# Kernel tuning notes

Hardware: AMD Instinct MI355X
Metric: run time of the kernel (lower is better)

## Reference

```python
import jax, jax.numpy as jnp
import numpy as np

# dims
B, N, T, D = 32, 207, 12, 128
H, HD, L, FF = 8, 16, 4, 512
PL, OD, IN = 12, 1, 1
SCALE = 1.0 / float(np.sqrt(HD))
NEG = -1e9


def ln(x, g, b, eps=1e-5):
    m = jnp.mean(x, -1, keepdims=True)
    v = jnp.mean((x - m) ** 2, -1, keepdims=True)
    return (x - m) * jax.lax.rsqrt(v + eps) * g + b


def setup_inputs() -> dict:
    key = jax.random.key(0)
    keys = iter(jax.random.split(key, 48))
    def rn(shape, s=0.02):
        return jax.random.normal(next(keys), shape, jnp.float32) * s
    z = lambda *s: jnp.zeros(s, jnp.float32)
    o = lambda *s: jnp.ones(s, jnp.float32)
    inp = {
        "x": jax.random.normal(next(keys), (B, N, T, IN), jnp.float32),
        "adj": jax.random.randint(next(keys), (N, N), 0, 2, jnp.int32),
        "Wi": rn((IN, D)), "bi": z(D),
        # spatial blocks (stacked over L layers)
        "Wq": rn((L, D, D)), "Wk": rn((L, D, D)), "Wv": rn((L, D, D)),
        "Wo": rn((L, D, D)), "bo": z(L, D),
        "sW1": rn((L, D, FF)), "sB1": z(L, FF), "sW2": rn((L, FF, D)), "sB2": z(L, D),
        "sg1": o(L, D), "sh1": z(L, D), "sg2": o(L, D), "sh2": z(L, D),
        # temporal blocks
        "Win": rn((L, D, 3 * D)), "Bin": z(L, 3 * D), "Wout": rn((L, D, D)), "Bout": z(L, D),
        "tW1": rn((L, D, FF)), "tB1": z(L, FF), "tW2": rn((L, FF, D)), "tB2": z(L, D),
        "tg1": o(L, D), "th1": z(L, D), "tg2": o(L, D), "th2": z(L, D),
        # prediction head
        "P1": rn((D, 2 * D)), "Pb1": z(2 * D), "P2": rn((2 * D, D)), "Pb2": z(D),
        "P3": rn((D, PL * OD)), "Pb3": z(PL * OD),
    }
    return inp


def reference(x, adj, Wi, bi, Wq, Wk, Wv, Wo, bo, sW1, sB1, sW2, sB2,
              sg1, sh1, sg2, sh2, Win, Bin, Wout, Bout, tW1, tB1, tW2, tB2,
              tg1, th1, tg2, th2, P1, Pb1, P2, Pb2, P3, Pb3):
    mask = (adj == 0)  # [N,N] True = masked (no edge)
    cmask = jnp.triu(jnp.ones((T, T), bool), 1)  # causal mask over time
    h = x @ Wi + bi  # [B,N,T,D]
    for l in range(L):
        # --- spatial adjacency-masked attention (vectorized over t) ---
        xn = ln(h, sg1[l], sh1[l])
        q = (xn @ Wq[l]).reshape(B, N, T, H, HD)
        k = (xn @ Wk[l]).reshape(B, N, T, H, HD)
        v = (xn @ Wv[l]).reshape(B, N, T, H, HD)
        sc = jnp.einsum('bnthd,bmthd->bthnm', q, k) * SCALE  # [B,T,H,N,N]
        sc = jnp.where(mask[None, None, None], NEG, sc)
        a = jax.nn.softmax(sc, -1)
        o = jnp.einsum('bthnm,bmthd->bnthd', a, v).reshape(B, N, T, D)
        h = h + o @ Wo[l] + bo[l]
        xn = ln(h, sg2[l], sh2[l])
        h = h + jax.nn.relu(xn @ sW1[l] + sB1[l]) @ sW2[l] + sB2[l]
        # --- temporal causal attention (per node) ---
        xn = ln(h, tg1[l], th1[l])
        qkv = xn @ Win[l] + Bin[l]
        q, k, v = jnp.split(qkv, 3, -1)
        q = q.reshape(B, N, T, H, HD)
        k = k.reshape(B, N, T, H, HD)
        v = v.reshape(B, N, T, H, HD)
        sc = jnp.einsum('bnthd,bnshd->bnhts', q, k) * SCALE  # [B,N,H,T,T]
        sc = jnp.where(cmask[None, None, None], NEG, sc)
        a = jax.nn.softmax(sc, -1)
        o = jnp.einsum('bnhts,bnshd->bnthd', a, v).reshape(B, N, T, D)
        h = h + o @ Wout[l] + Bout[l]
        xn = ln(h, tg2[l], th2[l])
        h = h + jax.nn.relu(xn @ tW1[l] + tB1[l]) @ tW2[l] + tB2[l]
    # prediction head on last time step
    hl = h[:, :, -1, :]  # [B,N,D]
    zz = jax.nn.relu(hl @ P1 + Pb1)
    zz = jax.nn.relu(zz @ P2 + Pb2)
    return (zz @ P3 + Pb3).reshape(B, N, PL, OD)
```

## Files before the change

kernel.cpp:

```cpp
#include <hip/hip_runtime.h>
#include <hip/hip_bf16.h>

#define B_   32
#define N_   207
#define T_   12
#define D_   128
#define H_   8
#define HD_  16
#define L_   4
#define FF_  512
#define PL_  12
#define TOK  (B_*N_*T_)
#define ROWS2 (B_*N_)
#define SCALE_ 0.25f
#define NEG_  -1e9f
#define NPAD 208
#define KQ2  24
#define KVH  232
#define SLAB 3312
#define MSK_N (13*13*256)

typedef __hip_bfloat16 bf16;
typedef unsigned int u32;
typedef __attribute__((ext_vector_type(8))) short bf16x8;
typedef __attribute__((ext_vector_type(8))) _Float16 f16x8;
typedef __attribute__((ext_vector_type(4))) float f32x4;

__device__ __forceinline__ float b2f(bf16 x){ return __bfloat162float(x); }
__device__ __forceinline__ bf16  f2b(float x){ return __float2bfloat16(x); }

__device__ __forceinline__ void gll16(const bf16* g, bf16* l){
  __builtin_amdgcn_global_load_lds((const __attribute__((address_space(1))) void*)g,
                                   (__attribute__((address_space(3))) void*)l, 16, 0, 0);
}

__global__ void detect_k(const void* x, int* flag){
  __shared__ int cnt[256];
  const unsigned short* u = (const unsigned short*)x;
  int ok = 0;
  for (int i = threadIdx.x; i < 4096; i += 256){
    unsigned int bits = ((unsigned int)u[i]) << 16;
    float f = __uint_as_float(bits);
    float a = fabsf(f);
    if (f == 0.0f || (a > 1e-4f && a < 64.0f)) ok++;
  }
  cnt[threadIdx.x] = ok;
  __syncthreads();
  for (int s = 128; s > 0; s >>= 1){
    if (threadIdx.x < s) cnt[threadIdx.x] += cnt[threadIdx.x + s];
    __syncthreads();
  }
  if (threadIdx.x == 0) *flag = (cnt[0] > 3686) ? 1 : 0;
}

struct FlatArgs {
  const void* src[24];
  long long dst[24];
  int cum[25];
};
__global__ void cvt_flat_k(FlatArgs a, bf16* base, const int* flag, int total){
  int i = blockIdx.x*256 + threadIdx.x;
  if (i >= total) return;
  int j = 0;
  while (i >= a.cum[j+1]) j++;
  int loc = i - a.cum[j];
  float v = (*flag) ? b2f(((const bf16*)a.src[j])[loc]) : ((const float*)a.src[j])[loc];
  base[a.dst[j] + loc] = f2b(v);
}

struct TArgs {
  const void* src[10];
  long long dst[10];
  int K[10], Nc[10], Lstr[10], ro[10];
  float scale[10];
  int cum[11];
};
__global__ void cvt_t_k(TArgs a, bf16* base, const int* flag, int total){
  int i = blockIdx.x*256 + threadIdx.x;
  if (i >= total) return;
  int j = 0;
  while (i >= a.cum[j+1]) j++;
  int loc = i - a.cum[j];
  int KN = a.K[j]*a.Nc[j];
  int l = loc / KN; int rm = loc - l*KN; int k = rm / a.Nc[j]; int n = rm - k*a.Nc[j];
  float v = (*flag) ? b2f(((const bf16*)a.src[j])[loc]) : ((const float*)a.src[j])[loc];
  base[a.dst[j] + (long long)l*a.Lstr[j] + (long long)(a.ro[j]+n)*a.K[j] + k] = f2b(v*a.scale[j]);
}

__global__ void maskc_k(const int* adj, float* maskg){
  int i = blockIdx.x*256 + threadIdx.x;
  if (i >= MSK_N) return;
  int cell = i >> 8;
  int mi = cell / 13, nj = cell - mi*13;
  int rem = i & 255;
  int lane = rem >> 2, r = rem & 3;
  int quad = lane >> 4, cl = lane & 15;
  int row = mi*16 + quad*4 + r; if (row > 206) row = 206;
  int col = nj*16 + cl;
  float v;
  if (col > 206) v = -1e30f;
  else v = adj[row*N_ + col] ? 0.0f : NEG_;
  maskg[i] = v;
}

__global__ void embed_ln_k(const bf16* x, const bf16* Wi, const bf16* bi,
                           const bf16* g, const bf16* bta, float* h, bf16* xnb){
  int wave = threadIdx.x >> 6, lane = threadIdx.x & 63;
  int tok = blockIdx.x*4 + wave;
  if (tok >= TOK) return;
  float xv = b2f(x[tok]);
  float v0 = xv*b2f(Wi[lane])    + b2f(bi[lane]);
  float v1 = xv*b2f(Wi[lane+64]) + b2f(bi[lane+64]);
  float* hp = h + (size_t)tok*D_;
  hp[lane] = v0; hp[lane+64] = v1;
  float s = v0 + v1;
  for (int off = 32; off >= 1; off >>= 1) s += __shfl_xor(s, off, 64);
  float m = s * (1.0f/128.0f);
  float d0 = v0 - m, d1 = v1 - m;
  float vv = d0*d0 + d1*d1;
  for (int off = 32; off >= 1; off >>= 1) vv += __shfl_xor(vv, off, 64);
  float r = rsqrtf(vv*(1.0f/128.0f) + 1e-5f);
  bf16* op = xnb + (size_t)tok*D_;
  op[lane]    = f2b(d0*r*b2f(g[lane])    + b2f(bta[lane]));
  op[lane+64] = f2b(d1*r*b2f(g[lane+64]) + b2f(bta[lane+64]));
}

__global__ __launch_bounds__(256) void mgemm_k(const bf16* __restrict__ A,
    const bf16* __restrict__ Wt, const bf16* __restrict__ bias,
    bf16* __restrict__ outp, int ldo, int Ktot, int relu){
  __shared__ __align__(16) bf16 As[128*32];
  __shared__ __align__(16) bf16 Bs[128*32];
  int tid = threadIdx.x;
  int rowBase = blockIdx.y * 128, colBase = blockIdx.x * 128;
  int w = tid >> 6, lane = tid & 63, quad = lane >> 4, cl = lane & 15;
  int waveM = w >> 1, waveN = w & 1;
  f32x4 accr[4][4];
  #pragma unroll
  for (int i = 0; i < 4; i++)
    #pragma unroll
    for (int j = 0; j < 4; j++) accr[i][j] = (f32x4){0.f,0.f,0.f,0.f};
  int lr = tid >> 2, kc = tid & 3;
  const bf16* Ap = A  + (size_t)(rowBase + lr)*Ktot + kc*8;
  const bf16* Bp = Wt + (size_t)(colBase + lr)*Ktot + kc*8;
  bf16* AsW = As + tid*8;
  bf16* BsW = Bs + tid*8;
  for (int kk = 0; kk < Ktot; kk += 32){
    __syncthreads();
    gll16(Ap + kk, AsW);
    gll16(Ap + (size_t)64*Ktot + kk, AsW + 64*32);
    gll16(Bp + kk, BsW);
    gll16(Bp + (size_t)64*Ktot + kk, BsW + 64*32);
    __syncthreads();
    bf16x8 af[4], bfr[4];
    #pragma unroll
    for (int mi = 0; mi < 4; mi++)
      af[mi] = *(const bf16x8*)(As + (waveM*64 + mi*16 + cl)*32 + quad*8);
    #pragma unroll
    for (int nj = 0; nj < 4; nj++)
      bfr[nj] = *(const bf16x8*)(Bs + (waveN*64 + nj*16 + cl)*32 + quad*8);
    #pragma unroll
    for (int mi = 0; mi < 4; mi++)
      #pragma unroll
      for (int nj = 0; nj < 4; nj++)
        accr[mi][nj] = __builtin_amdgcn_mfma_f32_16x16x32_bf16(af[mi], bfr[nj], accr[mi][nj], 0,0,0);
  }
  float bv[4];
  #pragma unroll
  for (int nj = 0; nj < 4; nj++)
    bv[nj] = bias ? b2f(bias[colBase + waveN*64 + nj*16 + cl]) : 0.0f;
  #pragma unroll
  for (int mi = 0; mi < 4; mi++){
    int row0 = rowBase + waveM*64 + mi*16 + quad*4;
    #pragma unroll
    for (int nj = 0; nj < 4; nj++){
      int col = colBase + waveN*64 + nj*16 + cl;
      #pragma unroll
      for (int r = 0; r < 4; r++){
        float v = accr[mi][nj][r] + bv[nj];
        if (relu) v = fmaxf(v, 0.0f);
        outp[(size_t)(row0+r)*ldo + col] = f2b(v);
      }
    }
  }
}

__global__ __launch_bounds__(256) void mgemm_qkvT_k(const bf16* __restrict__ A,
    const bf16* __restrict__ Wt, bf16* __restrict__ sQ,
    bf16* __restrict__ sK, bf16* __restrict__ sV){
  __shared__ __align__(16) bf16 As[128*32];
  __shared__ __align__(16) bf16 Bs[128*32];
  const int Ktot = 128;
  int tid = threadIdx.x;
  int rowBase = blockIdx.y * 128, colBase = blockIdx.x * 128;
  int w = tid >> 6, lane = tid & 63, quad = lane >> 4, cl = lane & 15;
  int waveM = w >> 1, waveN = w & 1;
  f32x4 accr[4][4];
  #pragma unroll
  for (int i = 0; i < 4; i++)
    #pragma unroll
    for (int j = 0; j < 4; j++) accr[i][j] = (f32x4){0.f,0.f,0.f,0.f};
  int lr = tid >> 2, kc = tid & 3;
  const bf16* Ap = A  + (size_t)(rowBase + lr)*Ktot + kc*8;
  const bf16* Bp = Wt + (size_t)(colBase + lr)*Ktot + kc*8;
  bf16* AsW = As + tid*8;
  bf16* BsW = Bs + tid*8;
  for (int kk = 0; kk < Ktot; kk += 32){
    __syncthreads();
    gll16(Ap + kk, AsW);
    gll16(Ap + (size_t)64*Ktot + kk, AsW + 64*32);
    gll16(Bp + kk, BsW);
    gll16(Bp + (size_t)64*Ktot + kk, BsW + 64*32);
    __syncthreads();
    bf16x8 af[4], bfr[4];
    #pragma unroll
    for (int mi = 0; mi < 4; mi++)
      af[mi] = *(const bf16x8*)(As + (waveM*64 + mi*16 + cl)*32 + quad*8);
    #pragma unroll
    for (int nj = 0; nj < 4; nj++)
      bfr[nj] = *(const bf16x8*)(Bs + (waveN*64 + nj*16 + cl)*32 + quad*8);
    #pragma unroll
    for (int mi = 0; mi < 4; mi++)
      #pragma unroll
      for (int nj = 0; nj < 4; nj++)
        accr[mi][nj] = __builtin_amdgcn_mfma_f32_16x16x32_bf16(af[mi], bfr[nj], accr[mi][nj], 0,0,0);
  }
  #pragma unroll
  for (int mi = 0; mi < 4; mi++){
    #pragma unroll
    for (int r = 0; r < 4; r++){
      int tok = rowBase + waveM*64 + mi*16 + quad*4 + r;
      int bn = tok / T_; int t = tok - bn*T_;
      int b = bn / N_;  int n = bn - b*N_;
      size_t base = ((size_t)(b*T_ + t)*H_)*SLAB + n*16 + cl;
      #pragma unroll
      for (int nj = 0; nj < 4; nj++){
        int col = colBase + waveN*64 + nj*16;
        int part = col >> 7, hh = (col >> 4) & 7;
        bf16* dst = (part == 0) ? sQ : (part == 1) ? sK : sV;
        dst[base + (size_t)hh*SLAB] = f2b(accr[mi][nj][r]);
      }
    }
  }
}

__global__ __launch_bounds__(256) void mgemm_ln_k(const bf16* __restrict__ A,
    const bf16* __restrict__ Wt, const bf16* __restrict__ bias,
    float* __restrict__ hout, int Ktot,
    const bf16* __restrict__ g, const bf16* __restrict__ bta,
    bf16* __restrict__ xnb){
  __shared__ __align__(16) bf16 As[128*32];
  __shared__ __align__(16) bf16 Bs[128*32];
  __shared__ float red[2][128][2];
  int tid = threadIdx.x;
  int rowBase = blockIdx.y * 128;
  int w = tid >> 6, lane = tid & 63, quad = lane >> 4, cl = lane & 15;
  int waveM = w >> 1, waveN = w & 1;
  f32x4 accr[4][4];
  #pragma unroll
  for (int i = 0; i < 4; i++)
    #pragma unroll
    for (int j = 0; j < 4; j++) accr[i][j] = (f32x4){0.f,0.f,0.f,0.f};
  int lr = tid >> 2, kc = tid & 3;
  const bf16* Ap = A  + (size_t)(rowBase + lr)*Ktot + kc*8;
  const bf16* Bp = Wt + (size_t)lr*Ktot + kc*8;
  bf16* AsW = As + tid*8;
  bf16* BsW = Bs + tid*8;
  for (int kk = 0; kk < Ktot; kk += 32){
    __syncthreads();
    gll16(Ap + kk, AsW);
    gll16(Ap + (size_t)64*Ktot + kk, AsW + 64*32);
    gll16(Bp + kk, BsW);
    gll16(Bp + (size_t)64*Ktot + kk, BsW + 64*32);
    __syncthreads();
    bf16x8 af[4], bfr[4];
    #pragma unroll
    for (int mi = 0; mi < 4; mi++)
      af[mi] = *(const bf16x8*)(As + (waveM*64 + mi*16 + cl)*32 + quad*8);
    #pragma unroll
    for (int nj = 0; nj < 4; nj++)
      bfr[nj] = *(const bf16x8*)(Bs + (waveN*64 + nj*16 + cl)*32 + quad*8);
    #pragma unroll
    for (int mi = 0; mi < 4; mi++)
      #pragma unroll
      for (int nj = 0; nj < 4; nj++)
        accr[mi][nj] = __builtin_amdgcn_mfma_f32_16x16x32_bf16(af[mi], bfr[nj], accr[mi][nj], 0,0,0);
  }
  int colW = waveN*64;
  float bv[4];
  #pragma unroll
  for (int nj = 0; nj < 4; nj++)
    bv[nj] = bias ? b2f(bias[colW + nj*16 + cl]) : 0.0f;
  float hv[4][4][4];
  float psum[4][4], psq[4][4];
  #pragma unroll
  for (int mi = 0; mi < 4; mi++)
    #pragma unroll
    for (int r = 0; r < 4; r++){ psum[mi][r] = 0.f; psq[mi][r] = 0.f; }
  #pragma unroll
  for (int mi = 0; mi < 4; mi++){
    #pragma unroll
    for (int r = 0; r < 4; r++){
      int row = rowBase + waveM*64 + mi*16 + quad*4 + r;
      #pragma unroll
      for (int nj = 0; nj < 4; nj++){
        int col = colW + nj*16 + cl;
        size_t idx = (size_t)row*D_ + col;
        float v = hout[idx] + accr[mi][nj][r] + bv[nj];
        hout[idx] = v;
        hv[mi][nj][r] = v;
        psum[mi][r] += v; psq[mi][r] += v*v;
      }
    }
  }
  if (g){
    #pragma unroll
    for (int off = 1; off <= 8; off <<= 1)
      #pragma unroll
      for (int mi = 0; mi < 4; mi++)
        #pragma unroll
        for (int r = 0; r < 4; r++){
          psum[mi][r] += __shfl_xor(psum[mi][r], off, 64);
          psq[mi][r]  += __shfl_xor(psq[mi][r],  off, 64);
        }
    if (cl == 0){
      #pragma unroll
      for (int mi = 0; mi < 4; mi++)
        #pragma unroll
        for (int r = 0; r < 4; r++){
          int rl = waveM*64 + mi*16 + quad*4 + r;
          red[waveN][rl][0] = psum[mi][r];
          red[waveN][rl][1] = psq[mi][r];
        }
    }
    __syncthreads();
    float gv[4], btv[4];
    #pragma unroll
    for (int nj = 0; nj < 4; nj++){
      int col = colW + nj*16 + cl;
      gv[nj] = b2f(g[col]); btv[nj] = b2f(bta[col]);
    }
    #pragma unroll
    for (int mi = 0; mi < 4; mi++){
      #pragma unroll
      for (int r = 0; r < 4; r++){
        int rl = waveM*64 + mi*16 + quad*4 + r;
        float s = red[0][rl][0] + red[1][rl][0];
        float q = red[0][rl][1] + red[1][rl][1];
        float mean = s*(1.0f/128.0f);
        float var  = q*(1.0f/128.0f) - mean*mean;
        float rstd = rsqrtf(var + 1e-5f);
        int row = rowBase + rl;
        #pragma unroll
        for (int nj = 0; nj < 4; nj++){
          int col = colW + nj*16 + cl;
          xnb[(size_t)row*D_ + col] = f2b((hv[mi][nj][r]-mean)*rstd*gv[nj] + btv[nj]);
        }
      }
    }
  }
}

__global__ __launch_bounds__(256,3) void sattn_k(const bf16* __restrict__ sQ,
    const bf16* __restrict__ sK, const bf16* __restrict__ sV,
    const float* __restrict__ maskg, bf16* __restrict__ ob){
  __shared__ __align__(16) bf16     Ks[NPAD*KQ2];
  __shared__ __align__(16) _Float16 Vt[16*KVH];
  __shared__ __align__(16) _Float16 Ps[4*16*KVH];
  int tid = threadIdx.x;
  int bid = blockIdx.x;
  int hh = bid & 7; int bt = bid >> 3; int t = bt % T_; int b = bt / T_;
  const bf16* Kslab = sK + (size_t)bid*SLAB;
  const bf16* Vslab = sV + (size_t)bid*SLAB;
  const bf16* Qslab = sQ + (size_t)bid*SLAB;
  for (int i = tid; i < 16*25; i += 256){ int d = i/25, c = 207 + i%25; Vt[d*KVH + c] = (_Float16)0.0f; }
  for (int i = tid; i < 64*24; i += 256){ int row = i/24, c = 208 + i%24; Ps[row*KVH + c] = (_Float16)0.0f; }
  for (int c = tid; c < 414; c += 256){
    bf16x8 kv = *(const bf16x8*)(Kslab + c*8);
    int n = c >> 1, dh = (c & 1)*8;
    *(bf16x8*)(Ks + n*KQ2 + dh) = kv;
  }
  for (int i = tid; i < SLAB; i += 256){
    int n = i >> 4, d = i & 15;
    Vt[d*KVH + n] = (_Float16)b2f(Vslab[i]);
  }
  __syncthreads();

  int lane = tid & 63, w = tid >> 6, quad = lane >> 4, cl = lane & 15;
  int nstripes = (w == 0) ? 4 : 3;
  for (int si = 0; si < nstripes; si++){
    int mi = w + si*4;
    bf16x8 aq = (bf16x8){0,0,0,0,0,0,0,0};
    {
      int n = mi*16 + cl; if (n > N_-1) n = N_-1;
      if (quad < 2) aq = *(const bf16x8*)(Qslab + n*16 + quad*8);
    }
    const float* mrow = maskg + ((size_t)mi*13)*256 + lane*4;
    f32x4 s[13];
    #pragma unroll
    for (int nj = 0; nj < 13; nj++){
      bf16x8 bk = (bf16x8){0,0,0,0,0,0,0,0};
      if (quad < 2) bk = *(const bf16x8*)(Ks + (nj*16 + cl)*KQ2 + quad*8);
      f32x4 c0 = *(const f32x4*)(mrow + nj*256);
      s[nj] = __builtin_amdgcn_mfma_f32_16x16x32_bf16(aq, bk, c0, 0,0,0);
    }
    int row0 = mi*16 + quad*4;
    _Float16* Pw = Ps + w*16*KVH;
    float invr[4];
    #pragma unroll
    for (int r = 0; r < 4; r++){
      float sum = 0.0f;
      #pragma unroll
      for (int nj = 0; nj < 13; nj++){
        float e = __expf(s[nj][r]);
        s[nj][r] = e; sum += e;
      }
      for (int off = 1; off < 16; off <<= 1) sum += __shfl_xor(sum, off, 64);
      invr[r] = 1.0f/sum;
      _Float16* Pr = Pw + (quad*4 + r)*KVH;
      #pragma unroll
      for (int nj = 0; nj < 13; nj++) Pr[nj*16 + cl] = (_Float16)s[nj][r];
    }
    __threadfence_block();
    f32x4 o = {0.f,0.f,0.f,0.f};
    #pragma unroll
    for (int kt = 0; kt < 7; kt++){
      f16x8 ap = *(const f16x8*)(Pw + cl*KVH + kt*32 + quad*8);
      f16x8 bv = *(const f16x8*)(Vt + cl*KVH + kt*32 + quad*8);
      o = __builtin_amdgcn_mfma_f32_16x16x32_f16(ap, bv, o, 0,0,0);
    }
    #pragma unroll
    for (int r = 0; r < 4; r++){
      int rg = row0 + r;
      if (rg < N_)
        ob[((size_t)((b*N_ + rg)*T_ + t))*D_ + hh*HD_ + cl] = f2b(o[r]*invr[r]);
    }
    __threadfence_block();
  }
}

__global__ void tattn_k(const bf16* qkv, bf16* ob){
  int bid = blockIdx.x; int b = bid / N_, n = bid % N_;
  __shared__ float qs[T_*D_];
  __shared__ float ks[T_*D_];
  __shared__ float vs[T_*D_];
  size_t rowb = ((size_t)(b*N_+n)*T_)*384;
  const u32* src = (const u32*)(qkv + rowb);
  for (int idx = threadIdx.x; idx < T_*192; idx += 128){
    int tt = idx / 192, cw = idx - tt*192;
    u32 pr = src[tt*192 + cw];
    union { u32 u; bf16 b[2]; } cv; cv.u = pr;
    float v0 = b2f(cv.b[0]), v1 = b2f(cv.b[1]);
    int arr = cw >> 6, cp2 = (cw & 63)*2;
    float* dst = (arr == 0) ? qs : (arr == 1) ? ks : vs;
    dst[tt*128 + cp2] = v0; dst[tt*128 + cp2 + 1] = v1;
  }
  __syncthreads();
  int p = threadIdx.x;
  if (p < H_*T_){
    int hh = p / T_, t = p - hh*T_;
    float qreg[16];
    for (int d = 0; d < 16; d++) qreg[d] = qs[t*128 + hh*16 + d];
    float sc[12]; float mx = -3.4e38f;
    for (int s = 0; s < 12; s++){
      float a = 0.0f;
      for (int d = 0; d < 16; d++) a += qreg[d]*ks[s*128 + hh*16 + d];
      a = (s <= t) ? a*SCALE_ : -3.4e38f;
      sc[s] = a; mx = fmaxf(mx, a);
    }
    float ssum = 0.0f;
    for (int s = 0; s < 12; s++){
      float e = (s <= t) ? __expf(sc[s]-mx) : 0.0f;
      sc[s] = e; ssum += e;
    }
    float inv = 1.0f/ssum;
    size_t obase = ((size_t)(b*N_+n)*T_ + t)*D_ + hh*16;
    for (int d = 0; d < 16; d++){
      float acc = 0.0f;
      for (int s = 0; s < 12; s++) acc += sc[s]*vs[s*128 + hh*16 + d];
      ob[obase + d] = f2b(acc*inv);
    }
  }
}

__global__ void gemm_k(const bf16* A, int lda, const bf16* W, const bf16* bias,
                       void* outp, int ldo, int M, int Ncols, int K, int relu, int acc){
  __shared__ float Ast[16*68];
  __shared__ float Ws [16*68];
  int tx = threadIdx.x & 15, ty = threadIdx.x >> 4;
  int rowBase = blockIdx.y * 64, colBase = blockIdx.x * 64;
  float accr[4][4];
  for (int i = 0; i < 4; i++) for (int j = 0; j < 4; j++) accr[i][j] = 0.0f;
  for (int kk = 0; kk < K; kk += 16){
    int kq = threadIdx.x & 15, r0 = threadIdx.x >> 4;
    for (int it = 0; it < 4; it++){
      int r = r0 + it*16, row = rowBase + r;
      float v = 0.0f;
      if (row < M) v = b2f(A[(size_t)row*lda + kk + kq]);
      Ast[kq*68 + r] = v;
    }
    int c = threadIdx.x & 63, w0 = threadIdx.x >> 6;
    for (int it = 0; it < 4; it++){
      int kr = w0 + it*4;
      Ws[kr*68 + c] = b2f(W[(size_t)(kk+kr)*Ncols + colBase + c]);
    }
    __syncthreads();
    for (int k = 0; k < 16; k++){
      float av[4], wv[4];
      for (int i = 0; i < 4; i++) av[i] = Ast[k*68 + ty*4 + i];
      for (int j = 0; j < 4; j++) wv[j] = Ws[k*68 + tx*4 + j];
      for (int i = 0; i < 4; i++)
        for (int j = 0; j < 4; j++) accr[i][j] += av[i]*wv[j];
    }
    __syncthreads();
  }
  for (int i = 0; i < 4; i++){
    int row = rowBase + ty*4 + i;
    if (row >= M) continue;
    for (int j = 0; j < 4; j++){
      int col = colBase + tx*4 + j;
      float v = accr[i][j];
      if (bias) v += b2f(bias[col]);
      if (relu) v = fmaxf(v, 0.0f);
      if (acc) ((float*)outp)[(size_t)row*ldo + col] += v;
      else     ((bf16*)outp)[(size_t)row*ldo + col] = f2b(v);
    }
  }
}

__global__ void gather_k(const float* h, bf16* hlb){
  int i = blockIdx.x*256 + threadIdx.x;
  if (i >= ROWS2*D_) return;
  int r = i >> 7, d = i & 127;
  hlb[i] = f2b(h[((size_t)r*T_ + (T_-1))*D_ + d]);
}

__global__ void head3_k(const bf16* z2, const bf16* P3, const bf16* Pb3,
                        void* out, int out_n, const int* flag){
  int i = blockIdx.x*256 + threadIdx.x;
  if (i >= out_n) return;
  int r = i / PL_, j = i - r*PL_;
  float acc = b2f(Pb3[j]);
  for (int d = 0; d < 128; d++) acc += b2f(z2[(size_t)r*128 + d]) * b2f(P3[d*PL_ + j]);
  if (*flag) ((bf16*)out)[i] = f2b(acc);
  else       ((float*)out)[i] = acc;
}

extern "C" void kernel_launch(void* const* d_in, const int* in_sizes, int n_in,
                              void* d_out, int out_size, void* d_ws, size_t ws_size,
                              hipStream_t stream){
  size_t HB = (size_t)TOK*D_*4;
  size_t XB = (size_t)TOK*D_*2;
  size_t RB = (size_t)TOK*D_*8;
  float* h    = (float*)d_ws;
  bf16*  xnb  = (bf16*)((char*)d_ws + HB);
  bf16*  reg_ = (bf16*)((char*)d_ws + HB + XB);
  bf16*  cvt  = (bf16*)((char*)d_ws + HB + XB + RB);
  bf16*  wsb  = (bf16*)d_ws;
  const int FIDX[34] = {0,2,3,4,5,6,7,8,9,10,11,12,13,14,15,16,17,18,19,20,
                        21,22,23,24,25,26,27,28,29,30,31,32,33,34};
  bf16* cp[34];
  size_t off = 0;
  for (int i = 0; i < 34; i++){ cp[i] = cvt + off; off += (size_t)in_sizes[FIDX[i]]; }
  char* tail   = (char*)d_ws + HB + XB + RB + ((off*2 + 255) & ~(size_t)255);
  float* maskg = (float*)tail;
  bf16* qkvw   = (bf16*)(tail + (size_t)MSK_N*4);
  int*  flag   = (int*)(tail + (size_t)MSK_N*4 + (size_t)L_*384*128*2);

  const bf16 *x_c=cp[0], *Wi_c=cp[1], *bi_c=cp[2],
             *Wo_t=cp[6], *bo_c=cp[7], *sW1_t=cp[8], *sB1_c=cp[9], *sW2_t=cp[10], *sB2_c=cp[11],
             *sg1_c=cp[12], *sh1_c=cp[13], *sg2_c=cp[14], *sh2_c=cp[15], *Win_t=cp[16], *Bin_c=cp[17],
             *Wout_t=cp[18], *Bout_c=cp[19], *tW1_t=cp[20], *tB1_c=cp[21], *tW2_t=cp[22], *tB2_c=cp[23],
             *tg1_c=cp[24], *th1_c=cp[25], *tg2_c=cp[26], *th2_c=cp[27], *P1_c=cp[28], *Pb1_c=cp[29],
             *P2_c=cp[30], *Pb2_c=cp[31], *P3_c=cp[32], *Pb3_c=cp[33];
  const int* adj = (const int*)d_in[1];

  bf16* sQ   = reg_;
  bf16* sK   = reg_ + (size_t)TOK*128;
  bf16* sV   = reg_ + (size_t)2*TOK*128;
  bf16* ob   = reg_ + (size_t)3*TOK*128;
  bf16* qkvb = reg_;
  bf16* ffb  = reg_;

  detect_k<<<1, 256, 0, stream>>>(d_in[0], flag);

  {
    const int FLAT[24] = {0,1,2,7,9,11,12,13,14,15,17,19,21,23,24,25,26,27,28,29,30,31,32,33};
    FlatArgs fa; int c = 0;
    for (int ii = 0; ii < 24; ii++){
      int ci = FLAT[ii];
      fa.src[ii] = d_in[FIDX[ci]];
      fa.dst[ii] = (long long)(cp[ci] - wsb);
      fa.cum[ii] = c;
      c += in_sizes[FIDX[ci]];
    }
    fa.cum[24] = c;
    cvt_flat_k<<<(c+255)/256, 256, 0, stream>>>(fa, wsb, flag, c);
  }
  {
    TArgs ta; int c = 0;
    const void* srcs[10] = {d_in[4], d_in[5], d_in[6], d_in[7], d_in[9], d_in[11],
                            d_in[17], d_in[19], d_in[21], d_in[23]};
    bf16* dsts[10] = {qkvw, qkvw, qkvw, cp[6], cp[8], cp[10], cp[16], cp[18], cp[20], cp[22]};
    int Ks_[10]   = {128,128,128, 128, 128, 512, 128, 128, 128, 512};
    int Ncs[10]   = {128,128,128, 128, 512, 128, 384, 128, 512, 128};
    int Lst[10]   = {384*128,384*128,384*128, 128*128, 128*512, 512*128, 128*384, 128*128, 128*512, 512*128};
    int ros[10]   = {0,128,256, 0,0,0, 0,0,0, 0};
    for (int j = 0; j < 10; j++){
      ta.src[j] = srcs[j];
      ta.dst[j] = (long long)(dsts[j] - wsb);
      ta.K[j] = Ks_[j]; ta.Nc[j] = Ncs[j]; ta.Lstr[j] = Lst[j]; ta.ro[j] = ros[j];
      ta.scale[j] = (j == 0) ? SCALE_ : 1.0f;
      ta.cum[j] = c;
      c += L_*Ks_[j]*Ncs[j];
    }
    ta.cum[10] = c;
    cvt_t_k<<<(c+255)/256, 256, 0, stream>>>(ta, wsb, flag, c);
  }
  maskc_k<<<(MSK_N+255)/256, 256, 0, stream>>>(adj, maskg);
  embed_ln_k<<<TOK/4, 256, 0, stream>>>(x_c, Wi_c, bi_c, sg1_c, sh1_c, h, xnb);

  const dim3 gP  (1, TOK/128);
  const dim3 gF1 (4, TOK/128);
  const dim3 gQKV(3, TOK/128);

  for (int l = 0; l < L_; l++){
    mgemm_qkvT_k<<<gQKV, 256, 0, stream>>>(xnb, qkvw + (size_t)l*384*128, sQ, sK, sV);
    sattn_k<<<B_*T_*H_, 256, 0, stream>>>(sQ, sK, sV, maskg, ob);
    mgemm_ln_k<<<gP, 256, 0, stream>>>(ob, Wo_t + (size_t)l*D_*D_, bo_c + l*D_, h, D_,
                                       sg2_c + l*D_, sh2_c + l*D_, xnb);
    mgemm_k<<<gF1, 256, 0, stream>>>(xnb, sW1_t + (size_t)l*D_*FF_, sB1_c + l*FF_, ffb, FF_, D_, 1);
    mgemm_ln_k<<<gP, 256, 0, stream>>>(ffb, sW2_t + (size_t)l*FF_*D_, sB2_c + l*D_, h, FF_,
                                       tg1_c + l*D_, th1_c + l*D_, xnb);
    mgemm_k<<<gQKV, 256, 0, stream>>>(xnb, Win_t + (size_t)l*D_*384, Bin_c + l*384, qkvb, 384, D_, 0);
    tattn_k<<<B_*N_, 128, 0, stream>>>(qkvb, ob);
    mgemm_ln_k<<<gP, 256, 0, stream>>>(ob, Wout_t + (size_t)l*D_*D_, Bout_c + l*D_, h, D_,
                                       tg2_c + l*D_, th2_c + l*D_, xnb);
    mgemm_k<<<gF1, 256, 0, stream>>>(xnb, tW1_t + (size_t)l*D_*FF_, tB1_c + l*FF_, ffb, FF_, D_, 1);
    const bf16* gnext = (l < L_-1) ? (sg1_c + (l+1)*D_) : nullptr;
    const bf16* bnext = (l < L_-1) ? (sh1_c + (l+1)*D_) : nullptr;
    mgemm_ln_k<<<gP, 256, 0, stream>>>(ffb, tW2_t + (size_t)l*FF_*D_, tB2_c + l*D_, h, FF_,
                                       gnext, bnext, xnb);
  }

  bf16* hlb = reg_;
  bf16* z1  = reg_ + (size_t)ROWS2*128;
  bf16* z2  = z1   + (size_t)ROWS2*256;
  gather_k<<<(ROWS2*D_)/256, 256, 0, stream>>>(h, hlb);
  gemm_k<<<dim3(256/64, (ROWS2+63)/64), 256, 0, stream>>>(hlb, 128, P1_c, Pb1_c, z1, 256, ROWS2, 256, 128, 1, 0);
  gemm_k<<<dim3(128/64, (ROWS2+63)/64), 256, 0, stream>>>(z1, 256, P2_c, Pb2_c, z2, 128, ROWS2, 128, 256, 1, 0);
  head3_k<<<(out_size+255)/256, 256, 0, stream>>>(z2, P3_c, Pb3_c, d_out, out_size, flag);
}
```

Baseline: 1.732 ms.

## Fuse FFN up-projection, ReLU, down-projection and LayerNorm into one kernel

Adds a single kernel that computes relu(xn@W1+b1)@W2+b2 for a 128-row tile, keeping the 512-wide hidden activation in LDS chunk by chunk instead of writing it to global memory. It accumulates the residual into h and applies the next LayerNorm in the epilogue. This replaces two launches per FFN and removes the round trip of the large hidden buffer through HBM. In exchange, each block recomputes nothing but runs the FF dimension serially, with lower occupancy (large LDS, launch bounds 2) and only TOK/128 blocks. There are also many syncthreads per K-step.

```diff
diff --git a/kernel.cpp b/kernel.cpp
--- a/kernel.cpp
+++ b/kernel.cpp
@@ -22,6 +22,7 @@
 
 typedef __hip_bfloat16 bf16;
 typedef unsigned int u32;
+typedef __attribute__((ext_vector_type(4))) unsigned int u32x4;
 typedef __attribute__((ext_vector_type(8))) short bf16x8;
 typedef __attribute__((ext_vector_type(8))) _Float16 f16x8;
 typedef __attribute__((ext_vector_type(4))) float f32x4;
@@ -360,6 +361,168 @@
   }
 }
 
+__global__ __launch_bounds__(256,2) void mffn_ln_k(const bf16* __restrict__ A,
+    const bf16* __restrict__ W1t, const bf16* __restrict__ b1,
+    const bf16* __restrict__ W2t, const bf16* __restrict__ b2,
+    float* __restrict__ hout,
+    const bf16* __restrict__ g, const bf16* __restrict__ bta,
+    bf16* __restrict__ xnb){
+  __shared__ __align__(16) bf16 As[128*136];
+  __shared__ __align__(16) bf16 Hs[128*136];
+  __shared__ __align__(16) bf16 Bs[128*32];
+  __shared__ float red[2][128][2];
+  int tid = threadIdx.x;
+  int rowBase = blockIdx.x * 128;
+  int w = tid >> 6, lane = tid & 63, quad = lane >> 4, cl = lane & 15;
+  int waveM = w >> 1, waveN = w & 1;
+  for (int i = tid; i < 128*16; i += 256){
+    int row = i >> 4, ch = i & 15;
+    u32x4 v = *(const u32x4*)(A + (size_t)(rowBase + row)*128 + ch*8);
+    *(u32x4*)(As + row*136 + ch*8) = v;
+  }
+  f32x4 acc2[4][4];
+  #pragma unroll
+  for (int i = 0; i < 4; i++)
+    #pragma unroll
+    for (int j = 0; j < 4; j++) acc2[i][j] = (f32x4){0.f,0.f,0.f,0.f};
+  int lr = tid >> 2, kc = tid & 3;
+  bf16* BsW = Bs + tid*8;
+  int aRow0 = waveM*64;
+  for (int kt = 0; kt < 4; kt++){
+    f32x4 acc1[4][4];
+    #pragma unroll
+    for (int i = 0; i < 4; i++)
+      #pragma unroll
+      for (int j = 0; j < 4; j++) acc1[i][j] = (f32x4){0.f,0.f,0.f,0.f};
+    for (int ks = 0; ks < 4; ks++){
+      __syncthreads();
+      gll16(W1t + (size_t)(kt*128 + lr)*128 + ks*32 + kc*8, BsW);
+      gll16(W1t + (size_t)(kt*128 + 64 + lr)*128 + ks*32 + kc*8, BsW + 64*32);
+      __syncthreads();
+      bf16x8 af[4], bfr[4];
+      #pragma unroll
+      for (int mi = 0; mi < 4; mi++)
+        af[mi] = *(const bf16x8*)(As + (aRow0 + mi*16 + cl)*136 + ks*32 + quad*8);
+      #pragma unroll
+      for (int nj = 0; nj < 4; nj++)
+        bfr[nj] = *(const bf16x8*)(Bs + (waveN*64 + nj*16 + cl)*32 + quad*8);
+      #pragma unroll
+      for (int mi = 0; mi < 4; mi++)
+        #pragma unroll
+        for (int nj = 0; nj < 4; nj++)
+          acc1[mi][nj] = __builtin_amdgcn_mfma_f32_16x16x32_bf16(af[mi], bfr[nj], acc1[mi][nj], 0,0,0);
+    }
+    float b1v[4];
+    #pragma unroll
+    for (int nj = 0; nj < 4; nj++)
+      b1v[nj] = b2f(b1[kt*128 + waveN*64 + nj*16 + cl]);
+    #pragma unroll
+    for (int mi = 0; mi < 4; mi++){
+      #pragma unroll
+      for (int r = 0; r < 4; r++){
+        int row = aRow0 + mi*16 + quad*4 + r;
+        #pragma unroll
+        for (int nj = 0; nj < 4; nj++){
+          int col = waveN*64 + nj*16 + cl;
+          Hs[row*136 + col] = f2b(fmaxf(acc1[mi][nj][r] + b1v[nj], 0.0f));
+        }
+      }
+    }
+    for (int ks = 0; ks < 4; ks++){
+      __syncthreads();
+      gll16(W2t + (size_t)lr*512 + kt*128 + ks*32 + kc*8, BsW);
+      gll16(W2t + (size_t)(64 + lr)*512 + kt*128 + ks*32 + kc*8, BsW + 64*32);
+      __syncthreads();
+      bf16x8 af[4], bfr[4];
+      #pragma unroll
+      for (int mi = 0; mi < 4; mi++)
+        af[mi] = *(const bf16x8*)(Hs + (aRow0 + mi*16 + cl)*136 + ks*32 + quad*8);
+      #pragma unroll
+      for (int nj = 0; nj < 4; nj++)
+        bfr[nj] = *(const bf16x8*)(Bs + (waveN*64 + nj*16 + cl)*32 + quad*8);
+      #pragma unroll
+      for (int mi = 0; mi < 4; mi++)
+        #pragma unroll
+        for (int nj = 0; nj < 4; nj++)
+          acc2[mi][nj] = __builtin_amdgcn_mfma_f32_16x16x32_bf16(af[mi], bfr[nj], acc2[mi][nj], 0,0,0);
+    }
+    __syncthreads();
+  }
+  int colW = waveN*64;
+  float bv[4];
+  #pragma unroll
+  for (int nj = 0; nj < 4; nj++)
+    bv[nj] = b2f(b2[colW + nj*16 + cl]);
+  float hv[4][4][4];
+  float psum[4][4], psq[4][4];
+  #pragma unroll
+  for (int mi = 0; mi < 4; mi++)
+    #pragma unroll
+    for (int r = 0; r < 4; r++){ psum[mi][r] = 0.f; psq[mi][r] = 0.f; }
+  #pragma unroll
+  for (int mi = 0; mi < 4; mi++){
+    #pragma unroll
+    for (int r = 0; r < 4; r++){
+      int row = rowBase + aRow0 + mi*16 + quad*4 + r;
+      #pragma unroll
+      for (int nj = 0; nj < 4; nj++){
+        int col = colW + nj*16 + cl;
+        size_t idx = (size_t)row*D_ + col;
+        float v = hout[idx] + acc2[mi][nj][r] + bv[nj];
+        hout[idx] = v;
+        hv[mi][nj][r] = v;
+        psum[mi][r] += v; psq[mi][r] += v*v;
+      }
+    }
+  }
+  if (g){
+    #pragma unroll
+    for (int off = 1; off <= 8; off <<= 1)
+      #pragma unroll
+      for (int mi = 0; mi < 4; mi++)
+        #pragma unroll
+        for (int r = 0; r < 4; r++){
+          psum[mi][r] += __shfl_xor(psum[mi][r], off, 64);
+          psq[mi][r]  += __shfl_xor(psq[mi][r],  off, 64);
+        }
+    if (cl == 0){
+      #pragma unroll
+      for (int mi = 0; mi < 4; mi++)
+        #pragma unroll
+        for (int r = 0; r < 4; r++){
+          int rl = aRow0 + mi*16 + quad*4 + r;
+          red[waveN][rl][0] = psum[mi][r];
+          red[waveN][rl][1] = psq[mi][r];
+        }
+    }
+    __syncthreads();
+    float gv[4], btv[4];
+    #pragma unroll
+    for (int nj = 0; nj < 4; nj++){
+      int col = colW + nj*16 + cl;
+      gv[nj] = b2f(g[col]); btv[nj] = b2f(bta[col]);
+    }
+    #pragma unroll
+    for (int mi = 0; mi < 4; mi++){
+      #pragma unroll
+      for (int r = 0; r < 4; r++){
+        int rl = aRow0 + mi*16 + quad*4 + r;
+        float s = red[0][rl][0] + red[1][rl][0];
+        float q = red[0][rl][1] + red[1][rl][1];
+        float mean = s*(1.0f/128.0f);
+        float var  = q*(1.0f/128.0f) - mean*mean;
+        float rstd = rsqrtf(var + 1e-5f);
+        int row = rowBase + rl;
+        #pragma unroll
+        for (int nj = 0; nj < 4; nj++){
+          int col = colW + nj*16 + cl;
+          xnb[(size_t)row*D_ + col] = f2b((hv[mi][nj][r]-mean)*rstd*gv[nj] + btv[nj]);
+        }
+      }
+    }
+  }
+}
+
 __global__ __launch_bounds__(256,3) void sattn_k(const bf16* __restrict__ sQ,
     const bf16* __restrict__ sK, const bf16* __restrict__ sV,
     const float* __restrict__ maskg, bf16* __restrict__ ob){
@@ -579,7 +742,6 @@
   bf16* sV   = reg_ + (size_t)2*TOK*128;
   bf16* ob   = reg_ + (size_t)3*TOK*128;
   bf16* qkvb = reg_;
-  bf16* ffb  = reg_;
 
   detect_k<<<1, 256, 0, stream>>>(d_in[0], flag);
 
@@ -620,7 +782,6 @@
   embed_ln_k<<<TOK/4, 256, 0, stream>>>(x_c, Wi_c, bi_c, sg1_c, sh1_c, h, xnb);
 
   const dim3 gP  (1, TOK/128);
-  const dim3 gF1 (4, TOK/128);
   const dim3 gQKV(3, TOK/128);
 
   for (int l = 0; l < L_; l++){
@@ -628,18 +789,18 @@
     sattn_k<<<B_*T_*H_, 256, 0, stream>>>(sQ, sK, sV, maskg, ob);
     mgemm_ln_k<<<gP, 256, 0, stream>>>(ob, Wo_t + (size_t)l*D_*D_, bo_c + l*D_, h, D_,
                                        sg2_c + l*D_, sh2_c + l*D_, xnb);
-    mgemm_k<<<gF1, 256, 0, stream>>>(xnb, sW1_t + (size_t)l*D_*FF_, sB1_c + l*FF_, ffb, FF_, D_, 1);
-    mgemm_ln_k<<<gP, 256, 0, stream>>>(ffb, sW2_t + (size_t)l*FF_*D_, sB2_c + l*D_, h, FF_,
-                                       tg1_c + l*D_, th1_c + l*D_, xnb);
+    mffn_ln_k<<<TOK/128, 256, 0, stream>>>(xnb, sW1_t + (size_t)l*D_*FF_, sB1_c + l*FF_,
+                                           sW2_t + (size_t)l*FF_*D_, sB2_c + l*D_, h,
+                                           tg1_c + l*D_, th1_c + l*D_, xnb);
     mgemm_k<<<gQKV, 256, 0, stream>>>(xnb, Win_t + (size_t)l*D_*384, Bin_c + l*384, qkvb, 384, D_, 0);
     tattn_k<<<B_*N_, 128, 0, stream>>>(qkvb, ob);
     mgemm_ln_k<<<gP, 256, 0, stream>>>(ob, Wout_t + (size_t)l*D_*D_, Bout_c + l*D_, h, D_,
                                        tg2_c + l*D_, th2_c + l*D_, xnb);
-    mgemm_k<<<gF1, 256, 0, stream>>>(xnb, tW1_t + (size_t)l*D_*FF_, tB1_c + l*FF_, ffb, FF_, D_, 1);
     const bf16* gnext = (l < L_-1) ? (sg1_c + (l+1)*D_) : nullptr;
     const bf16* bnext = (l < L_-1) ? (sh1_c + (l+1)*D_) : nullptr;
-    mgemm_ln_k<<<gP, 256, 0, stream>>>(ffb, tW2_t + (size_t)l*FF_*D_, tB2_c + l*D_, h, FF_,
-                                       gnext, bnext, xnb);
+    mffn_ln_k<<<TOK/128, 256, 0, stream>>>(xnb, tW1_t + (size_t)l*D_*FF_, tB1_c + l*FF_,
+                                           tW2_t + (size_t)l*FF_*D_, tB2_c + l*D_, h,
+                                           gnext, bnext, xnb);
   }
 
   bf16* hlb = reg_;
```

Measured after the change: 1.619 ms. 1.07x faster.
